# Kernel tuning notes

Hardware: AMD Instinct MI355X
Metric: run time of the kernel (lower is better)

## Reference

```python
import jax, jax.numpy as jnp
import numpy as np

N = 50000
IN_CH = 512
OUT_CH = 512
DEG = 32
E = N * DEG


def setup_inputs() -> dict:
    key = jax.random.key(0)
    kx, kwc, kwn, kb, ke = jax.random.split(key, 5)
    x = jax.random.normal(kx, (N, IN_CH), dtype=jnp.float32)
    bound = 1.0 / np.sqrt(IN_CH)
    wc = jax.random.uniform(kwc, (IN_CH, OUT_CH), minval=-bound, maxval=bound, dtype=jnp.float32)
    wn = jax.random.uniform(kwn, (IN_CH, OUT_CH), minval=-bound, maxval=bound, dtype=jnp.float32)
    bias = jax.random.uniform(kb, (OUT_CH,), minval=-bound, maxval=bound, dtype=jnp.float32)
    # Every node appears as a source exactly DEG times -> no empty-neighborhood NaNs.
    src = jnp.repeat(jnp.arange(N, dtype=jnp.int64), DEG)
    dst = jax.random.randint(ke, (E,), 0, N, dtype=jnp.int64)
    edge_index = jnp.stack([src, dst], axis=0)  # [2, E]
    return {"x": x, "wc": wc, "wn": wn, "bias": bias, "edge_index": edge_index}


def reference(x, wc, wn, bias, edge_index):
    # alpha = x @ wc ; beta = x @ wn
    alpha = x @ wc                       # [N, out]
    beta = x @ wn                        # [N, out]
    src, dst = edge_index[0], edge_index[1]
    # gamma[n] = mean_{e: src[e]==n} beta[dst[e]]
    sums = jax.ops.segment_sum(beta[dst], src, num_segments=x.shape[0])          # [N, out]
    counts = jax.ops.segment_sum(jnp.ones_like(src, dtype=beta.dtype), src,
                                 num_segments=x.shape[0])                        # [N]
    gamma = sums / counts[:, None]
    return alpha + gamma + bias
```

## Files before the change

kernel.cpp:

```cpp
#include <hip/hip_runtime.h>


#define M_ROWS 50000
#define DEG 32
#define NE (M_ROWS * DEG)
#define SLICE_DW 800000

typedef short s16x8 __attribute__((ext_vector_type(8)));
typedef float f32x4 __attribute__((ext_vector_type(4)));
typedef float f32x2 __attribute__((ext_vector_type(2)));
typedef unsigned int u32x2 __attribute__((ext_vector_type(2)));

__device__ __forceinline__ unsigned short f2bf(float f) {
  union { float f; unsigned int u; } c; c.f = f;
  unsigned int u = c.u;
  u += 0x7fffu + ((u >> 16) & 1u);
  return (unsigned short)(u >> 16);
}

__device__ __forceinline__ float bfhi(unsigned int u) {
  return __uint_as_float(u & 0xffff0000u);
}
__device__ __forceinline__ float bflo(unsigned int u) {
  return __uint_as_float(u << 16);
}

__device__ __forceinline__ void gl_lds16(const void* g, void* l) {
  __builtin_amdgcn_global_load_lds(
      (const __attribute__((address_space(1))) unsigned int*)g,
      (__attribute__((address_space(3))) unsigned int*)l, 16, 0, 0);
}

__global__ __launch_bounds__(256) void k_convert_x(
    const float* __restrict__ x, unsigned short* __restrict__ xb) {
  const size_t base = ((size_t)blockIdx.x * 256 + threadIdx.x) * 8;
  const float4 a = *(const float4*)(x + base);
  const float4 b = *(const float4*)(x + base + 4);
  union { unsigned short u[8]; uint4 v; } p;
  p.u[0] = f2bf(a.x); p.u[1] = f2bf(a.y); p.u[2] = f2bf(a.z); p.u[3] = f2bf(a.w);
  p.u[4] = f2bf(b.x); p.u[5] = f2bf(b.y); p.u[6] = f2bf(b.z); p.u[7] = f2bf(b.w);
  *(uint4*)(xb + base) = p.v;
}

__global__ __launch_bounds__(256) void k_convert_w(
    const float* __restrict__ wc, const float* __restrict__ wn,
    unsigned short* __restrict__ wt) {
  const int k = blockIdx.x;
  const int n4 = threadIdx.x * 4;
  const float* src = (n4 < 512) ? (wc + (size_t)k * 512 + n4)
                                : (wn + (size_t)k * 512 + (n4 - 512));
  const float4 v = *(const float4*)src;
  wt[(size_t)(n4 + 0) * 512 + k] = f2bf(v.x);
  wt[(size_t)(n4 + 1) * 512 + k] = f2bf(v.y);
  wt[(size_t)(n4 + 2) * 512 + k] = f2bf(v.z);
  wt[(size_t)(n4 + 3) * 512 + k] = f2bf(v.w);
}

__global__ __launch_bounds__(256) void k_convert_dst(
    const int* __restrict__ dst, unsigned short* __restrict__ d16) {
  const size_t base = ((size_t)blockIdx.x * 256 + threadIdx.x) * 8;
  if (base >= NE) return;
  const int4 a = *(const int4*)(dst + base);
  const int4 b = *(const int4*)(dst + base + 4);
  union { unsigned short u[8]; uint4 v; } p;
  p.u[0] = (unsigned short)a.x; p.u[1] = (unsigned short)a.y;
  p.u[2] = (unsigned short)a.z; p.u[3] = (unsigned short)a.w;
  p.u[4] = (unsigned short)b.x; p.u[5] = (unsigned short)b.y;
  p.u[6] = (unsigned short)b.z; p.u[7] = (unsigned short)b.w;
  *(uint4*)(d16 + base) = p.v;
}

__global__ __launch_bounds__(256) void k_gemm(
    const unsigned short* __restrict__ xb,
    const unsigned short* __restrict__ wt,
    const float* __restrict__ bias,
    unsigned short* __restrict__ alphab,
    unsigned char* __restrict__ betaf8) {
  __shared__ __attribute__((aligned(16))) unsigned short As[128 * 64];
  __shared__ __attribute__((aligned(16))) unsigned short Bs[128 * 64];

  const int tid = threadIdx.x;
  const int g = blockIdx.x;
  int mt, nt;
  if (g < 3072) {
    const int c = g & 7, j = g >> 3;
    nt = j & 7; mt = (j >> 3) * 8 + c;
  } else {
    const int r = g - 3072;
    mt = 384 + (r >> 3); nt = r & 7;
  }
  const int n0 = nt * 128;
  const int m0 = mt * 128;

  const int wv = tid >> 6;
  const int l = tid & 63;
  const int lm = l & 15;
  const int quad = l >> 4;
  const int mb = (wv >> 1) * 64;
  const int nb = (wv & 1) * 64;

  size_t aofs[4], bofs[4];
  int ldst[4];
#pragma unroll
  for (int s = 0; s < 4; ++s) {
    const int c = s * 256 + tid;
    const int row = c >> 3;
    const int seg = c & 7;
    const int sg = seg ^ (row & 7);
    int am = m0 + row; if (am >= M_ROWS) am = M_ROWS - 1;
    aofs[s] = (size_t)am * 512 + sg * 8;
    bofs[s] = (size_t)(n0 + row) * 512 + sg * 8;
    ldst[s] = (s * 256 + (tid & ~63)) * 16;
  }

  f32x4 acc[4][4];
#pragma unroll
  for (int i = 0; i < 4; ++i)
#pragma unroll
    for (int j = 0; j < 4; ++j) acc[i][j] = (f32x4)(0.0f);

  for (int kt = 0; kt < 8; ++kt) {
    const int k0 = kt * 64;
    __syncthreads();
#pragma unroll
    for (int s = 0; s < 4; ++s) {
      gl_lds16(xb + aofs[s] + k0, (char*)As + ldst[s]);
      gl_lds16(wt + bofs[s] + k0, (char*)Bs + ldst[s]);
    }
    __syncthreads();

#pragma unroll
    for (int h = 0; h < 2; ++h) {
      s16x8 af[4], bfr[4];
#pragma unroll
      for (int i = 0; i < 4; ++i) {
        const int R = mb + 16 * i + lm;
        af[i] = *(const s16x8*)&As[R * 64 + (((h * 4 + quad) ^ (R & 7)) << 3)];
      }
#pragma unroll
      for (int j = 0; j < 4; ++j) {
        const int R = nb + 16 * j + lm;
        bfr[j] = *(const s16x8*)&Bs[R * 64 + (((h * 4 + quad) ^ (R & 7)) << 3)];
      }
#pragma unroll
      for (int i = 0; i < 4; ++i)
#pragma unroll
        for (int j = 0; j < 4; ++j)
          acc[i][j] = __builtin_amdgcn_mfma_f32_16x16x32_bf16(
              af[i], bfr[j], acc[i][j], 0, 0, 0);
    }
  }

  const bool isAlpha = (n0 < 512);
  const int grp64 = (n0 + nb) >> 6;
  float b4[4];
#pragma unroll
  for (int j = 0; j < 4; ++j)
    b4[j] = isAlpha ? bias[n0 + nb + 16 * j + lm] : 0.0f;

  if (isAlpha) {
    unsigned int* ap = (unsigned int*)alphab;
#pragma unroll
    for (int i = 0; i < 4; ++i) {
#pragma unroll
      for (int r = 0; r < 4; ++r) {
        const int m = m0 + mb + 16 * i + quad * 4 + r;
        if (m < M_ROWS) {
          u32x2 v;
          v.x = (unsigned int)f2bf(acc[i][0][r] + b4[0]) |
                ((unsigned int)f2bf(acc[i][1][r] + b4[1]) << 16);
          v.y = (unsigned int)f2bf(acc[i][2][r] + b4[2]) |
                ((unsigned int)f2bf(acc[i][3][r] + b4[3]) << 16);
          *(u32x2*)(ap + (size_t)m * 256 + grp64 * 32 + 2 * lm) = v;
        }
      }
    }
  } else {
    unsigned int* bp = (unsigned int*)betaf8 + (size_t)(grp64 - 8) * SLICE_DW;
#pragma unroll
    for (int i = 0; i < 4; ++i) {
#pragma unroll
      for (int r = 0; r < 4; ++r) {
        const int m = m0 + mb + 16 * i + quad * 4 + r;
        if (m < M_ROWS) {
          int p = __builtin_amdgcn_cvt_pk_fp8_f32(acc[i][0][r], acc[i][1][r], 0, false);
          p = __builtin_amdgcn_cvt_pk_fp8_f32(acc[i][2][r], acc[i][3][r], p, true);
          bp[(size_t)m * 16 + lm] = (unsigned int)p;
        }
      }
    }
  }
}

template <typename IT>
__global__ __launch_bounds__(256, 8) void k_gather(
    const IT* __restrict__ dst, const unsigned int* __restrict__ beta32,
    const unsigned int* __restrict__ alpha32, float* __restrict__ out) {
  const int b = blockIdx.x;
  const int phase = b & 7;
  const int tid = threadIdx.x;
  const int w = tid >> 6;
  const int l = tid & 63;
  const int lm = l & 15;
  const int abase = (l & 48) << 2;
  const unsigned lmoff = (unsigned)lm * 4u;
  const char* base = (const char*)(beta32 + (size_t)phase * SLICE_DW);
  const float s = 1.0f / 32.0f;
  const int nsub = w * 2 + ((l >> 5) & 1);

  for (int q = b >> 3; q < 6250; q += 256) {
    const int vstage = (int)(unsigned)__builtin_nontemporal_load(
        dst + (size_t)q * 256 + tid);

    f32x2 s01 = (f32x2)(0.0f), s23 = (f32x2)(0.0f);
#pragma unroll
    for (int h = 0; h < 2; ++h) {
      unsigned int bb[8];
#pragma unroll
      for (int e = 0; e < 8; ++e) {
        const int row = __builtin_amdgcn_ds_bpermute(
            abase + ((h * 8 + e) << 2), vstage);
        bb[e] = *(const unsigned int*)(base + (((unsigned)row << 6) + lmoff));
      }
#pragma unroll
      for (int e = 0; e < 8; ++e) {
        s01 += __builtin_amdgcn_cvt_pk_f32_fp8(bb[e], false);
        s23 += __builtin_amdgcn_cvt_pk_f32_fp8(bb[e], true);
      }
    }

    s01.x += __shfl_xor(s01.x, 16, 64);
    s01.y += __shfl_xor(s01.y, 16, 64);
    s23.x += __shfl_xor(s23.x, 16, 64);
    s23.y += __shfl_xor(s23.y, 16, 64);

    if (!(l & 16)) {
      const int node = q * 8 + nsub;
      const u32x2 av = __builtin_nontemporal_load(
          (const u32x2*)(alpha32 + (size_t)node * 256 + phase * 32) + lm);
      float* ob = out + (size_t)node * 512 + phase * 64;
      __builtin_nontemporal_store(bflo(av.x) + s01.x * s, ob + lm);
      __builtin_nontemporal_store(bfhi(av.x) + s01.y * s, ob + 16 + lm);
      __builtin_nontemporal_store(bflo(av.y) + s23.x * s, ob + 32 + lm);
      __builtin_nontemporal_store(bfhi(av.y) + s23.y * s, ob + 48 + lm);
    }
  }
}

extern "C" void kernel_launch(void* const* d_in, const int* in_sizes, int n_in,
                              void* d_out, int out_size, void* d_ws, size_t ws_size,
                              hipStream_t stream) {
  const float* x    = (const float*)d_in[0];
  const float* wc   = (const float*)d_in[1];
  const float* wn   = (const float*)d_in[2];
  const float* bias = (const float*)d_in[3];
  const int*   ei   = (const int*)d_in[4];
  float* out = (float*)d_out;

  char* ws = (char*)d_ws;
  unsigned short* xb     = (unsigned short*)ws;
  unsigned short* wt     = (unsigned short*)(ws + 51200000);
  unsigned short* alphab = (unsigned short*)(ws + 52248576);
  unsigned char*  betaf8 = (unsigned char*)(ws + 103448576);
  unsigned short* d16    = (unsigned short*)(ws + 129048576);
  const bool u16ok = (ws_size >= (size_t)129048576 + 3200000);

  k_convert_x<<<12500, 256, 0, stream>>>(x, xb);
  k_convert_w<<<512, 256, 0, stream>>>(wc, wn, wt);
  if (u16ok) k_convert_dst<<<782, 256, 0, stream>>>(ei + NE, d16);
  k_gemm<<<3128, 256, 0, stream>>>(xb, wt, bias, alphab, betaf8);
  if (u16ok) {
    k_gather<unsigned short><<<2048, 256, 0, stream>>>(
        d16, (const unsigned int*)betaf8, (const unsigned int*)alphab, out);
  } else {
    k_gather<int><<<2048, 256, 0, stream>>>(
        ei + NE, (const unsigned int*)betaf8, (const unsigned int*)alphab, out);
  }
}
```

Measured before the change: 386.9 us.

## Widen fp8 beta slices to 128-byte rows and use one block per node quartet

Changes the fp8 beta layout from eight 64-byte column slices to four 128-byte paired slices, so each gathered neighbor row is fetched as a full 128-byte line by 32 lanes. The gather kernel drops its grid-stride loop and launches one block per 4 nodes and slice pair, handling 16 edges per half-wave and reducing across halves with a 32-lane shuffle. This is meant to raise per-request gather efficiency and cut the number of slice passes over the index array. The cost is a much larger grid and a changed cache-locality pattern across the four slices.

```diff
diff --git a/kernel.cpp b/kernel.cpp
--- a/kernel.cpp
+++ b/kernel.cpp
@@ -4,7 +4,7 @@
 #define M_ROWS 50000
 #define DEG 32
 #define NE (M_ROWS * DEG)
-#define SLICE_DW 800000
+#define PAIR_DW (M_ROWS * 32)
 
 typedef short s16x8 __attribute__((ext_vector_type(8)));
 typedef float f32x4 __attribute__((ext_vector_type(4)));
@@ -176,7 +176,9 @@
       }
     }
   } else {
-    unsigned int* bp = (unsigned int*)betaf8 + (size_t)(grp64 - 8) * SLICE_DW;
+    const int pr = grp64 - 8;
+    unsigned int* bp = (unsigned int*)betaf8 + (size_t)(pr >> 1) * PAIR_DW;
+    const int g16 = (pr & 1) * 16;
 #pragma unroll
     for (int i = 0; i < 4; ++i) {
 #pragma unroll
@@ -185,7 +187,7 @@
         if (m < M_ROWS) {
           int p = __builtin_amdgcn_cvt_pk_fp8_f32(acc[i][0][r], acc[i][1][r], 0, false);
           p = __builtin_amdgcn_cvt_pk_fp8_f32(acc[i][2][r], acc[i][3][r], p, true);
-          bp[(size_t)m * 16 + lm] = (unsigned int)p;
+          bp[(size_t)m * 32 + g16 + lm] = (unsigned int)p;
         }
       }
     }
@@ -193,57 +195,58 @@
 }
 
 template <typename IT>
-__global__ __launch_bounds__(256, 8) void k_gather(
+__global__ __launch_bounds__(256) void k_gather(
     const IT* __restrict__ dst, const unsigned int* __restrict__ beta32,
     const unsigned int* __restrict__ alpha32, float* __restrict__ out) {
   const int b = blockIdx.x;
-  const int phase = b & 7;
+  const int pair = b & 3;
+  const int q = b >> 2;
   const int tid = threadIdx.x;
   const int w = tid >> 6;
   const int l = tid & 63;
-  const int lm = l & 15;
-  const int abase = (l & 48) << 2;
-  const unsigned lmoff = (unsigned)lm * 4u;
-  const char* base = (const char*)(beta32 + (size_t)phase * SLICE_DW);
-  const float s = 1.0f / 32.0f;
-  const int nsub = w * 2 + ((l >> 5) & 1);
-
-  for (int q = b >> 3; q < 6250; q += 256) {
-    const int vstage = (int)(unsigned)__builtin_nontemporal_load(
-        dst + (size_t)q * 256 + tid);
-
-    f32x2 s01 = (f32x2)(0.0f), s23 = (f32x2)(0.0f);
-#pragma unroll
-    for (int h = 0; h < 2; ++h) {
-      unsigned int bb[8];
-#pragma unroll
-      for (int e = 0; e < 8; ++e) {
-        const int row = __builtin_amdgcn_ds_bpermute(
-            abase + ((h * 8 + e) << 2), vstage);
-        bb[e] = *(const unsigned int*)(base + (((unsigned)row << 6) + lmoff));
-      }
-#pragma unroll
-      for (int e = 0; e < 8; ++e) {
-        s01 += __builtin_amdgcn_cvt_pk_f32_fp8(bb[e], false);
-        s23 += __builtin_amdgcn_cvt_pk_f32_fp8(bb[e], true);
-      }
-    }
-
-    s01.x += __shfl_xor(s01.x, 16, 64);
-    s01.y += __shfl_xor(s01.y, 16, 64);
-    s23.x += __shfl_xor(s23.x, 16, 64);
-    s23.y += __shfl_xor(s23.y, 16, 64);
-
-    if (!(l & 16)) {
-      const int node = q * 8 + nsub;
-      const u32x2 av = __builtin_nontemporal_load(
-          (const u32x2*)(alpha32 + (size_t)node * 256 + phase * 32) + lm);
-      float* ob = out + (size_t)node * 512 + phase * 64;
-      __builtin_nontemporal_store(bflo(av.x) + s01.x * s, ob + lm);
-      __builtin_nontemporal_store(bfhi(av.x) + s01.y * s, ob + 16 + lm);
-      __builtin_nontemporal_store(bflo(av.y) + s23.x * s, ob + 32 + lm);
-      __builtin_nontemporal_store(bfhi(av.y) + s23.y * s, ob + 48 + lm);
-    }
+  const int lm2 = l & 31;
+  const int node = q * 4 + w;
+
+  const int vstage = (int)(unsigned)__builtin_nontemporal_load(
+      dst + (size_t)node * 32 + lm2);
+
+  const char* base = (const char*)(beta32 + (size_t)pair * PAIR_DW);
+  const int abase = (l & 32) * 6;
+  const unsigned lmoff = (unsigned)lm2 * 4u;
+
+  f32x2 s01 = (f32x2)(0.0f), s23 = (f32x2)(0.0f);
+#pragma unroll
+  for (int h = 0; h < 2; ++h) {
+    unsigned int bb[8];
+#pragma unroll
+    for (int e = 0; e < 8; ++e) {
+      const int row = __builtin_amdgcn_ds_bpermute(
+          abase + ((h * 8 + e) << 2), vstage);
+      bb[e] = *(const unsigned int*)(base + (((unsigned)row << 7) + lmoff));
+    }
+#pragma unroll
+    for (int e = 0; e < 8; ++e) {
+      s01 += __builtin_amdgcn_cvt_pk_f32_fp8(bb[e], false);
+      s23 += __builtin_amdgcn_cvt_pk_f32_fp8(bb[e], true);
+    }
+  }
+
+  s01.x += __shfl_xor(s01.x, 32, 64);
+  s01.y += __shfl_xor(s01.y, 32, 64);
+  s23.x += __shfl_xor(s23.x, 32, 64);
+  s23.y += __shfl_xor(s23.y, 32, 64);
+
+  if (l < 32) {
+    const int g = l >> 4;
+    const int lm = l & 15;
+    const u32x2 av = __builtin_nontemporal_load(
+        (const u32x2*)(alpha32 + (size_t)node * 256 + (pair * 2 + g) * 32) + lm);
+    const float s = 1.0f / 32.0f;
+    float* ob = out + (size_t)node * 512 + pair * 128 + g * 64;
+    __builtin_nontemporal_store(bflo(av.x) + s01.x * s, ob + lm);
+    __builtin_nontemporal_store(bfhi(av.x) + s01.y * s, ob + 16 + lm);
+    __builtin_nontemporal_store(bflo(av.y) + s23.x * s, ob + 32 + lm);
+    __builtin_nontemporal_store(bfhi(av.y) + s23.y * s, ob + 48 + lm);
   }
 }
 
@@ -270,10 +273,10 @@
   if (u16ok) k_convert_dst<<<782, 256, 0, stream>>>(ei + NE, d16);
   k_gemm<<<3128, 256, 0, stream>>>(xb, wt, bias, alphab, betaf8);
   if (u16ok) {
-    k_gather<unsigned short><<<2048, 256, 0, stream>>>(
+    k_gather<unsigned short><<<50000, 256, 0, stream>>>(
         d16, (const unsigned int*)betaf8, (const unsigned int*)alphab, out);
   } else {
-    k_gather<int><<<2048, 256, 0, stream>>>(
+    k_gather<int><<<50000, 256, 0, stream>>>(
         ei + NE, (const unsigned int*)betaf8, (const unsigned int*)alphab, out);
   }
 }
```

Result: faster. 348.6 us (-9.9%).
